# Optimization experiments

Hardware: AMD Instinct MI355X
Metric: run time of the kernel (lower is better)

The kernel has to match this reference:

```python
import jax, jax.numpy as jnp
import numpy as np

NUM_GRAPHS = 128
EPS = 1e-5


def _instance_norm(x, seg):
    # per-graph (segment) normalization over rows, per channel; affine=False (PyG default)
    ones = jnp.ones((x.shape[0],), x.dtype)
    cnt = jnp.maximum(jax.ops.segment_sum(ones, seg, num_segments=NUM_GRAPHS), 1.0)[:, None]
    mean = jax.ops.segment_sum(x, seg, num_segments=NUM_GRAPHS) / cnt
    ex2 = jax.ops.segment_sum(x * x, seg, num_segments=NUM_GRAPHS) / cnt
    var = jnp.maximum(ex2 - mean * mean, 0.0)
    return (x - mean[seg]) * jax.lax.rsqrt(var[seg] + EPS)


def setup_inputs() -> dict:
    key = jax.random.key(0)
    ks = jax.random.split(key, 6)
    N, E, H = 100_000, 1_600_000, 64
    emb = jax.random.normal(ks[0], (N, H), jnp.float32)
    edge_index = jax.random.randint(ks[1], (2, E), 0, N)
    batch = jnp.sort(jax.random.randint(ks[2], (N,), 0, NUM_GRAPHS))
    s = lambda fan: 1.0 / np.sqrt(fan)
    # MLP layers [2H, 4H, H, 1]
    W1 = jax.random.uniform(ks[3], (2 * H, 4 * H), jnp.float32, -s(2 * H), s(2 * H))
    b1 = jnp.zeros((4 * H,), jnp.float32)
    W2 = jax.random.uniform(ks[4], (4 * H, H), jnp.float32, -s(4 * H), s(4 * H))
    b2 = jnp.zeros((H,), jnp.float32)
    W3 = jax.random.uniform(ks[5], (H, 1), jnp.float32, -s(H), s(H))
    b3 = jnp.zeros((1,), jnp.float32)
    return dict(emb=emb, edge_index=edge_index, batch=batch,
                W1=W1, b1=b1, W2=W2, b2=b2, W3=W3, b3=b3)


def reference(emb, edge_index, batch, W1, b1, W2, b2, W3, b3):
    col, row = edge_index[0], edge_index[1]
    # edge-wise gather + concat: [E, 2H]
    f12 = jnp.concatenate([emb[col], emb[row]], axis=-1)
    seg = batch[col]  # graph id per edge
    h = jax.nn.relu(_instance_norm(f12 @ W1 + b1, seg))   # [E, 4H]
    h = jax.nn.relu(_instance_norm(h @ W2 + b2, seg))     # [E, H]
    att_log_logits = h @ W3 + b3                          # [E, 1]
    return att_log_logits
```

## Files before the change

### kernel.cpp

```cpp
#include <hip/hip_runtime.h>
#include <hip/hip_bf16.h>

#define NSEG 128
#define H64 64
#define C1 256
#define K1 128
#define C2 64
#define EPSV 1e-5f
#define NWG 256

typedef __attribute__((ext_vector_type(8))) short bf16x8;
typedef __attribute__((ext_vector_type(16))) float f32x16;
typedef __attribute__((ext_vector_type(4))) unsigned int u32x4;

struct BTrue  { static constexpr bool value = true; };
struct BFalse { static constexpr bool value = false; };

__device__ __forceinline__ unsigned short f2bf(float f){
  unsigned int x = __float_as_uint(f);
  x += 0x7fffu + ((x >> 16) & 1u);
  return (unsigned short)(x >> 16);
}
__device__ __forceinline__ float bf2f(unsigned short u){
  return __uint_as_float(((unsigned int)u) << 16);
}
__device__ __forceinline__ unsigned pkbf(float lo, float hi){
  unsigned r;
  asm("v_cvt_pk_bf16_f32 %0, %1, %2" : "=v"(r) : "v"(lo), "v"(hi));
  return r;
}
__device__ __forceinline__ bf16x8 mk8(unsigned a, unsigned b, unsigned c, unsigned d){
  u32x4 t = {a, b, c, d};
  return __builtin_bit_cast(bf16x8, t);
}
__device__ __forceinline__ int xcd_swz(int bid, int nwg){
  int q = nwg >> 3, r = nwg & 7;
  int x = bid & 7, o = bid >> 3;
  return (x < r ? x * (q + 1) : r * (q + 1) + (x - r) * q) + o;
}

__global__ void k_cvt_emb(const float* __restrict__ src, unsigned short* __restrict__ dst, int n4){
  int i = blockIdx.x * blockDim.x + threadIdx.x;
  if (i >= n4) return;
  float4 v = ((const float4*)src)[i];
  unsigned int a = (unsigned int)f2bf(v.x) | ((unsigned int)f2bf(v.y) << 16);
  unsigned int b = (unsigned int)f2bf(v.z) | ((unsigned int)f2bf(v.w) << 16);
  ((uint2*)dst)[i] = make_uint2(a, b);
}

__global__ void k_cvt_w(const float* __restrict__ W1, const float* __restrict__ W2,
                        unsigned short* __restrict__ W1T, unsigned short* __restrict__ W2T){
  int i = blockIdx.x * blockDim.x + threadIdx.x;
  if (i < C1 * K1){
    int c = i >> 7, k = i & 127;
    W1T[i] = f2bf(W1[k * C1 + c]);
  } else {
    int j = i - C1 * K1;
    if (j < C2 * C1){
      int c = j >> 8, k = j & 255;
      W2T[j] = f2bf(W2[k * C2 + c]);
    }
  }
}

__global__ void k_hist(const int* __restrict__ col, const int* __restrict__ batch,
                       int* __restrict__ segE, int* __restrict__ cnt, int E){
  __shared__ int h[NSEG];
  for (int i = threadIdx.x; i < NSEG; i += blockDim.x) h[i] = 0;
  __syncthreads();
  int stride = gridDim.x * blockDim.x;
  for (int e = blockIdx.x * blockDim.x + threadIdx.x; e < E; e += stride){
    int s = batch[col[e]];
    segE[e] = s;
    atomicAdd(&h[s], 1);
  }
  __syncthreads();
  for (int i = threadIdx.x; i < NSEG; i += blockDim.x)
    if (h[i]) atomicAdd(&cnt[i], h[i]);
}

__global__ void k_scan(const int* __restrict__ cnt, int* __restrict__ cursor,
                       float* __restrict__ cntf){
  if (threadIdx.x == 0){
    int acc = 0;
    for (int i = 0; i < NSEG; i++){ cursor[i] = acc; acc += cnt[i]; }
  }
  if (threadIdx.x < NSEG){
    int c = cnt[threadIdx.x];
    cntf[threadIdx.x] = (float)(c > 0 ? c : 1);
  }
}

__global__ void k_scatter(const int* __restrict__ segE, const int* __restrict__ ei,
                          int* __restrict__ cursor, int* __restrict__ perm,
                          int* __restrict__ segS, int* __restrict__ ecol, int* __restrict__ erow,
                          int* __restrict__ invp, int E, int epb){
  __shared__ int h[NSEG];
  __shared__ int base[NSEG];
  int b0 = blockIdx.x * epb;
  int b1 = b0 + epb < E ? b0 + epb : E;
  for (int i = threadIdx.x; i < NSEG; i += blockDim.x) h[i] = 0;
  __syncthreads();
  for (int e = b0 + threadIdx.x; e < b1; e += blockDim.x) atomicAdd(&h[segE[e]], 1);
  __syncthreads();
  for (int i = threadIdx.x; i < NSEG; i += blockDim.x)
    base[i] = h[i] ? atomicAdd(&cursor[i], h[i]) : 0;
  __syncthreads();
  for (int i = threadIdx.x; i < NSEG; i += blockDim.x) h[i] = 0;
  __syncthreads();
  for (int e = b0 + threadIdx.x; e < b1; e += blockDim.x){
    int s = segE[e];
    int p = base[s] + atomicAdd(&h[s], 1);
    perm[p] = e; segS[p] = s;
    ecol[p] = ei[e]; erow[p] = ei[(size_t)E + e];
    invp[e] = p;
  }
}

__global__ void __launch_bounds__(1024, 4)
k_stats1(const unsigned short* __restrict__ ebf, const unsigned short* __restrict__ W1T,
         const int* __restrict__ ecol, const int* __restrict__ erow, const int* __restrict__ segS,
         float* __restrict__ sum1, float* __restrict__ sq1, int NWT, int E, int T)
{
  __shared__ __align__(16) char wl[65536];
  {
    #pragma unroll
    for (int j = 0; j < 4; j++){
      int i = threadIdx.x + j * 1024;
      int r = i >> 4, u = i & 15;
      u32x4 v = *(const u32x4*)(W1T + (size_t)r * K1 + u * 8);
      *(u32x4*)(wl + r * 256 + ((u ^ (r & 15)) << 4)) = v;
    }
  }
  __syncthreads();

  const int lane = threadIdx.x & 63, w = threadIdx.x >> 6;
  const int g = lane >> 5, l31 = lane & 31;
  const int bid = xcd_swz(blockIdx.x, NWG);
  const int wt0 = (bid * 16 + w) * T;
  float psum[8] = {0,0,0,0,0,0,0,0}, psq[8] = {0,0,0,0,0,0,0,0};
  int cur = -1;

  auto flush = [&](int seg){
    if (seg < 0) return;
    #pragma unroll
    for (int nt = 0; nt < 8; nt++){
      float sv = psum[nt] + __shfl_xor(psum[nt], 32);
      float qv = psq[nt]  + __shfl_xor(psq[nt], 32);
      if (lane < 32){
        atomicAdd(&sum1[seg * C1 + nt * 32 + l31], sv);
        atomicAdd(&sq1 [seg * C1 + nt * 32 + l31], qv);
      }
      psum[nt] = 0.f; psq[nt] = 0.f;
    }
  };

  auto ld3 = [&](int wt, int& a, int& r, int& s){
    int e = wt * 32 + l31;
    int ec = e < E ? e : E - 1;
    a = ecol[ec]; r = erow[ec]; s = segS[ec];
  };

  int cA, rA, sg;
  if (wt0 < NWT) ld3(wt0, cA, rA, sg);

  for (int it = 0; it < T; ++it){
    int wt = wt0 + it;
    if (wt >= NWT) break;
    const int p0 = wt * 32;
    int nA, nR, nS;
    const bool hv = (it + 1 < T) && (wt + 1 < NWT);
    if (hv) ld3(wt + 1, nA, nR, nS);

    bf16x8 fa[8];
    #pragma unroll
    for (int kk = 0; kk < 8; kk++){
      int off = (kk & 3) * 16 + g * 8;
      fa[kk] = *(const bf16x8*)(ebf + (size_t)(kk < 4 ? cA : rA) * H64 + off);
    }

    int sA = __builtin_amdgcn_readfirstlane(__shfl(sg, 0));
    int sB = __builtin_amdgcn_readfirstlane(__shfl(sg, 31));
    bool uni = (sA == sB) && (p0 + 32 <= E);
    if (uni && sA != cur){ flush(cur); cur = sA; }
    if (!uni){ flush(cur); cur = -1; }

    #pragma unroll 1
    for (int np = 0; np < 4; np++){
      const int nt0 = 2 * np, nt1 = 2 * np + 1;
      f32x16 a0, a1;
      #pragma unroll
      for (int r = 0; r < 16; r++){ a0[r] = 0.f; a1[r] = 0.f; }
      const int rw0 = nt0 * 32 + l31, rw1 = nt1 * 32 + l31;
      __builtin_amdgcn_s_setprio(1);
      #pragma unroll
      for (int kk = 0; kk < 8; kk++){
        bf16x8 b0 = *(const bf16x8*)(wl + rw0 * 256 + (((2 * kk + g) ^ (rw0 & 15)) << 4));
        bf16x8 b1 = *(const bf16x8*)(wl + rw1 * 256 + (((2 * kk + g) ^ (rw1 & 15)) << 4));
        a0 = __builtin_amdgcn_mfma_f32_32x32x16_bf16(fa[kk], b0, a0, 0, 0, 0);
        a1 = __builtin_amdgcn_mfma_f32_32x32x16_bf16(fa[kk], b1, a1, 0, 0, 0);
      }
      __builtin_amdgcn_s_setprio(0);
      if (uni){
        float t0 = 0.f, q0 = 0.f, t1 = 0.f, q1 = 0.f;
        #pragma unroll
        for (int r = 0; r < 16; r++){
          t0 += a0[r]; q0 += a0[r] * a0[r];
          t1 += a1[r]; q1 += a1[r] * a1[r];
        }
        psum[nt0] += t0; psq[nt0] += q0;
        psum[nt1] += t1; psq[nt1] += q1;
      } else {
        for (int s = sA; s <= sB; s++){
          float t0 = 0.f, q0 = 0.f, t1 = 0.f, q1 = 0.f;
          #pragma unroll
          for (int r = 0; r < 16; r++){
            int c = (r & 3) + 8 * (r >> 2) + 4 * g;
            bool ok = (__shfl(sg, c) == s) && (p0 + c < E);
            float v0 = ok ? a0[r] : 0.f;
            float v1 = ok ? a1[r] : 0.f;
            t0 += v0; q0 += v0 * v0;
            t1 += v1; q1 += v1 * v1;
          }
          float s0 = t0 + __shfl_xor(t0, 32);
          float qq0 = q0 + __shfl_xor(q0, 32);
          float s1 = t1 + __shfl_xor(t1, 32);
          float qq1 = q1 + __shfl_xor(q1, 32);
          if (lane < 32){
            atomicAdd(&sum1[s * C1 + nt0 * 32 + l31], s0);
            atomicAdd(&sq1 [s * C1 + nt0 * 32 + l31], qq0);
            atomicAdd(&sum1[s * C1 + nt1 * 32 + l31], s1);
            atomicAdd(&sq1 [s * C1 + nt1 * 32 + l31], qq1);
          }
        }
      }
    }
    if (hv){ cA = nA; rA = nR; sg = nS; }
  }
  flush(cur);
}

__global__ void k_fin(const float* __restrict__ sum, const float* __restrict__ sq,
                      const float* __restrict__ cntf,
                      float* __restrict__ sc, float* __restrict__ sh, int C){
  int i = blockIdx.x * blockDim.x + threadIdx.x;
  if (i >= NSEG * C) return;
  int s = i / C;
  float c = cntf[s];
  float m = sum[i] / c;
  float v = fmaxf(sq[i] / c - m * m, 0.f);
  float inv = rsqrtf(v + EPSV);
  sc[i] = inv;
  sh[i] = -m * inv;
}

template<int MODE>
__global__ void __launch_bounds__(1024, 4)
k_mid(const unsigned short* __restrict__ ebf, const unsigned short* __restrict__ W1T,
      const unsigned short* __restrict__ W2T,
      const int* __restrict__ ecol, const int* __restrict__ erow,
      const int* __restrict__ segS, const int* __restrict__ perm,
      const float* __restrict__ sc1, const float* __restrict__ sh1,
      float* __restrict__ sum2, float* __restrict__ sq2,
      unsigned int* __restrict__ y2u,
      const float* __restrict__ sc2, const float* __restrict__ sh2,
      const float* __restrict__ W3, const float* __restrict__ b3,
      float* __restrict__ out, int NWT, int E, int T)
{
  __shared__ __align__(16) char wl[98304];
  __shared__ __align__(16) float scsh[16][512];
  {
    #pragma unroll
    for (int j = 0; j < 4; j++){
      int i = threadIdx.x + j * 1024;
      int r = i >> 4, u = i & 15;
      u32x4 v = *(const u32x4*)(W1T + (size_t)r * K1 + u * 8);
      *(u32x4*)(wl + r * 256 + ((u ^ (r & 15)) << 4)) = v;
    }
    #pragma unroll
    for (int j = 0; j < 2; j++){
      int i = threadIdx.x + j * 1024;
      int r = i >> 5, u = i & 31;
      u32x4 v = *(const u32x4*)(W2T + (size_t)r * C1 + u * 8);
      *(u32x4*)(wl + 65536 + r * 512 + ((u ^ (r & 31)) << 4)) = v;
    }
  }
  __syncthreads();

  const int lane = threadIdx.x & 63, w = threadIdx.x >> 6;
  const int g = lane >> 5, l31 = lane & 31;
  const int bid = xcd_swz(blockIdx.x, NWG);
  const int wt0 = (bid * 16 + w) * T;

  float b3v = 0.f;
  if (MODE == 2) b3v = b3[0];
  int wseg = -1;

  auto body = [&](auto uni_c, const bf16x8* fbp, int sgn, f32x16* acc2){
    constexpr bool UNI = decltype(uni_c)::value;
    #pragma unroll 1
    for (int mt = 0; mt < 8; mt++){
      f32x16 a1;
      #pragma unroll
      for (int r = 0; r < 16; r++) a1[r] = 0.f;
      const int rw = mt * 32 + l31;
      __builtin_amdgcn_s_setprio(1);
      #pragma unroll
      for (int kk = 0; kk < 8; kk++){
        bf16x8 wa = *(const bf16x8*)(wl + rw * 256 + (((2 * kk + g) ^ (rw & 15)) << 4));
        a1 = __builtin_amdgcn_mfma_f32_32x32x16_bf16(wa, fbp[kk], a1, 0, 0, 0);
      }
      __builtin_amdgcn_s_setprio(0);
      unsigned pk_[8];
      #pragma unroll
      for (int rq = 0; rq < 4; rq++){
        float4 sc, sh;
        if constexpr (UNI){
          sc = *(const float4*)(&scsh[w][mt * 32 + rq * 8 + 4 * g]);
          sh = *(const float4*)(&scsh[w][256 + mt * 32 + rq * 8 + 4 * g]);
        } else {
          sc = *(const float4*)(sc1 + sgn * C1 + mt * 32 + rq * 8 + 4 * g);
          sh = *(const float4*)(sh1 + sgn * C1 + mt * 32 + rq * 8 + 4 * g);
        }
        float h0 = fmaxf(fmaf(a1[rq * 4 + 0], sc.x, sh.x), 0.f);
        float h1 = fmaxf(fmaf(a1[rq * 4 + 1], sc.y, sh.y), 0.f);
        float h2 = fmaxf(fmaf(a1[rq * 4 + 2], sc.z, sh.z), 0.f);
        float h3 = fmaxf(fmaf(a1[rq * 4 + 3], sc.w, sh.w), 0.f);
        pk_[rq * 2 + 0] = pkbf(h0, h1);
        pk_[rq * 2 + 1] = pkbf(h2, h3);
      }
      asm("v_permlane32_swap_b32 %0, %1" : "+v"(pk_[0]), "+v"(pk_[2]));
      asm("v_permlane32_swap_b32 %0, %1" : "+v"(pk_[1]), "+v"(pk_[3]));
      asm("v_permlane32_swap_b32 %0, %1" : "+v"(pk_[4]), "+v"(pk_[6]));
      asm("v_permlane32_swap_b32 %0, %1" : "+v"(pk_[5]), "+v"(pk_[7]));
      bf16x8 bf0 = mk8(pk_[0], pk_[1], pk_[2], pk_[3]);
      bf16x8 bf1 = mk8(pk_[4], pk_[5], pk_[6], pk_[7]);
      __builtin_amdgcn_s_setprio(1);
      #pragma unroll
      for (int ct = 0; ct < 2; ct++){
        int rb = ct * 32 + l31;
        bf16x8 wb0 = *(const bf16x8*)(wl + 65536 + rb * 512 + (((4 * mt + g) ^ (rb & 31)) << 4));
        bf16x8 wb1 = *(const bf16x8*)(wl + 65536 + rb * 512 + (((4 * mt + 2 + g) ^ (rb & 31)) << 4));
        acc2[ct] = __builtin_amdgcn_mfma_f32_32x32x16_bf16(wb0, bf0, acc2[ct], 0, 0, 0);
        acc2[ct] = __builtin_amdgcn_mfma_f32_32x32x16_bf16(wb1, bf1, acc2[ct], 0, 0, 0);
      }
      __builtin_amdgcn_s_setprio(0);
    }
  };

  auto ld3 = [&](int wt, int& a, int& r, int& s){
    int e = wt * 32 + l31;
    int ec = e < E ? e : E - 1;
    a = ecol[ec]; r = erow[ec]; s = segS[ec];
  };

  int cA, rA, sg;
  if (wt0 < NWT) ld3(wt0, cA, rA, sg);

  for (int it = 0; it < T; ++it){
    int wt = wt0 + it;
    if (wt >= NWT) break;
    const int p0 = wt * 32;
    int nA, nR, nS;
    const bool hv = (it + 1 < T) && (wt + 1 < NWT);
    if (hv) ld3(wt + 1, nA, nR, nS);

    int e0 = p0 + l31;
    bool v0 = e0 < E;

    bf16x8 fb[8];
    #pragma unroll
    for (int kk = 0; kk < 8; kk++){
      int off = (kk & 3) * 16 + g * 8;
      fb[kk] = *(const bf16x8*)(ebf + (size_t)(kk < 4 ? cA : rA) * H64 + off);
    }

    int sA = __builtin_amdgcn_readfirstlane(__shfl(sg, 0));
    int sB = __builtin_amdgcn_readfirstlane(__shfl(sg, 31));
    const bool uni = (sA == sB) && (p0 + 32 <= E);

    if (uni && sA != wseg){
      float4 s4 = *(const float4*)(sc1 + sA * C1 + lane * 4);
      float4 h4 = *(const float4*)(sh1 + sA * C1 + lane * 4);
      *(float4*)(&scsh[w][lane * 4]) = s4;
      *(float4*)(&scsh[w][256 + lane * 4]) = h4;
      wseg = sA;
    }

    f32x16 acc2[2];
    #pragma unroll
    for (int ct = 0; ct < 2; ct++)
      #pragma unroll
      for (int r = 0; r < 16; r++) acc2[ct][r] = 0.f;

    if (uni) body(BTrue{},  fb, sg, acc2);
    else     body(BFalse{}, fb, sg, acc2);

    if constexpr (MODE == 0){
      if (v0){
        unsigned* yp = y2u + (size_t)e0 * 32;
        #pragma unroll
        for (int ct = 0; ct < 2; ct++)
          #pragma unroll
          for (int rq = 0; rq < 4; rq++){
            uint2 pv;
            pv.x = pkbf(acc2[ct][rq * 4 + 0], acc2[ct][rq * 4 + 1]);
            pv.y = pkbf(acc2[ct][rq * 4 + 2], acc2[ct][rq * 4 + 3]);
            *(uint2*)(yp + ct * 16 + rq * 4 + 2 * g) = pv;
          }
      }
      for (int s = sA; s <= sB; s++){
        #pragma unroll
        for (int ct = 0; ct < 2; ct++)
          #pragma unroll
          for (int r = 0; r < 16; r++){
            float x = (v0 && sg == s) ? acc2[ct][r] : 0.f;
            float vs = x, vq = x * x;
            #pragma unroll
            for (int off = 1; off < 32; off <<= 1){
              vs += __shfl_xor(vs, off);
              vq += __shfl_xor(vq, off);
            }
            if (l31 == 0){
              int c2 = ct * 32 + (r & 3) + 8 * (r >> 2) + 4 * g;
              atomicAdd(&sum2[s * C2 + c2], vs);
              atomicAdd(&sq2 [s * C2 + c2], vq);
            }
          }
      }
    } else if constexpr (MODE == 1){
      for (int s = sA; s <= sB; s++){
        #pragma unroll
        for (int ct = 0; ct < 2; ct++)
          #pragma unroll
          for (int r = 0; r < 16; r++){
            float x = (v0 && sg == s) ? acc2[ct][r] : 0.f;
            float vs = x, vq = x * x;
            #pragma unroll
            for (int off = 1; off < 32; off <<= 1){
              vs += __shfl_xor(vs, off);
              vq += __shfl_xor(vq, off);
            }
            if (l31 == 0){
              int c2 = ct * 32 + (r & 3) + 8 * (r >> 2) + 4 * g;
              atomicAdd(&sum2[s * C2 + c2], vs);
              atomicAdd(&sq2 [s * C2 + c2], vq);
            }
          }
      }
    } else {
      float acc = 0.f;
      #pragma unroll
      for (int ct = 0; ct < 2; ct++)
        #pragma unroll
        for (int rq = 0; rq < 4; rq++){
          float4 sc = *(const float4*)(sc2 + sg * C2 + ct * 32 + rq * 8 + 4 * g);
          float4 sh = *(const float4*)(sh2 + sg * C2 + ct * 32 + rq * 8 + 4 * g);
          float4 wq = *(const float4*)(W3 + ct * 32 + rq * 8 + 4 * g);
          acc = fmaf(fmaxf(fmaf(acc2[ct][rq * 4 + 0], sc.x, sh.x), 0.f), wq.x, acc);
          acc = fmaf(fmaxf(fmaf(acc2[ct][rq * 4 + 1], sc.y, sh.y), 0.f), wq.y, acc);
          acc = fmaf(fmaxf(fmaf(acc2[ct][rq * 4 + 2], sc.z, sh.z), 0.f), wq.z, acc);
          acc = fmaf(fmaxf(fmaf(acc2[ct][rq * 4 + 3], sc.w, sh.w), 0.f), wq.w, acc);
        }
      acc += __shfl_xor(acc, 32);
      if (g == 0 && v0) out[perm[e0]] = acc + b3v;
    }
    if (hv){ cA = nA; rA = nR; sg = nS; }
  }
}

__global__ void k_out(const unsigned short* __restrict__ y2, const int* __restrict__ segS,
                      const float* __restrict__ sc2, const float* __restrict__ sh2,
                      const float* __restrict__ W3, const float* __restrict__ b3,
                      float* __restrict__ tmp, int E)
{
  const int lane = threadIdx.x & 63;
  const int wid = (blockIdx.x * blockDim.x + threadIdx.x) >> 6;
  const int nw = (gridDim.x * blockDim.x) >> 6;
  const int es = lane >> 3;
  const int cp = (lane & 7) * 8;
  float w3r[8];
  #pragma unroll
  for (int j = 0; j < 8; j++) w3r[j] = W3[cp + j];
  const float b3v = b3[0];
  for (long base = (long)wid * 8; base < E; base += (long)nw * 8){
    int pos = (int)base + es;
    float a = 0.f;
    if (pos < E){
      bf16x8 v = *(const bf16x8*)(y2 + (size_t)pos * C2 + cp);
      int s = segS[pos];
      const float* scp = sc2 + s * C2 + cp;
      const float* shp = sh2 + s * C2 + cp;
      #pragma unroll
      for (int j = 0; j < 8; j++){
        float hv = fmaxf(fmaf(bf2f((unsigned short)v[j]), scp[j], shp[j]), 0.f);
        a = fmaf(hv, w3r[j], a);
      }
    }
    a += __shfl_xor(a, 1); a += __shfl_xor(a, 2); a += __shfl_xor(a, 4);
    if ((lane & 7) == 0 && pos < E) tmp[pos] = a + b3v;
  }
}

__global__ void k_remap(const float* __restrict__ tmp, const int* __restrict__ invp,
                        float* __restrict__ out, int E)
{
  int stride = gridDim.x * blockDim.x;
  for (int e = blockIdx.x * blockDim.x + threadIdx.x; e < E; e += stride)
    out[e] = tmp[invp[e]];
}

extern "C" void kernel_launch(void* const* d_in, const int* in_sizes, int n_in,
                              void* d_out, int out_size, void* d_ws, size_t ws_size,
                              hipStream_t stream)
{
  const float* emb   = (const float*)d_in[0];
  const int*   ei    = (const int*)d_in[1];
  const int*   batch = (const int*)d_in[2];
  const float* W1    = (const float*)d_in[3];
  const float* W2    = (const float*)d_in[5];
  const float* W3    = (const float*)d_in[7];
  const float* b3    = (const float*)d_in[8];
  float* out = (float*)d_out;
  const int E = in_sizes[1] / 2;
  const int N = in_sizes[0] / H64;
  const int NWT = (E + 31) / 32;

  char* ws = (char*)d_ws;
  size_t o = 0;
  auto al = [&](size_t b){ size_t r = o; o = (o + b + 255) & ~((size_t)255); return r; };
  size_t o_ebf  = al((size_t)N * H64 * 2);
  size_t o_w1t  = al((size_t)C1 * K1 * 2);
  size_t o_w2t  = al((size_t)C2 * C1 * 2);
  size_t o_perm = al((size_t)E * 4);
  size_t o_segS = al((size_t)E * 4);
  size_t o_ecol = al((size_t)E * 4);
  size_t o_erow = al((size_t)E * 4);
  size_t o_invp = al((size_t)E * 4);
  size_t o_cnt  = al(NSEG * 4);
  size_t o_cur  = al(NSEG * 4);
  size_t o_cntf = al(NSEG * 4);
  size_t o_sum1 = al((size_t)NSEG * C1 * 4);
  size_t o_sq1  = al((size_t)NSEG * C1 * 4);
  size_t o_sum2 = al((size_t)NSEG * C2 * 4);
  size_t o_sq2  = al((size_t)NSEG * C2 * 4);
  size_t o_sc1  = al((size_t)NSEG * C1 * 4);
  size_t o_sh1  = al((size_t)NSEG * C1 * 4);
  size_t o_sc2  = al((size_t)NSEG * C2 * 4);
  size_t o_sh2  = al((size_t)NSEG * C2 * 4);
  size_t o_segE = al((size_t)E * 4);
  size_t o_y2   = o_segE;
  size_t need_full = o_segE + (size_t)E * C2 * 2;
  const bool full = ws_size >= need_full;

  unsigned short* ebf = (unsigned short*)(ws + o_ebf);
  unsigned short* W1T = (unsigned short*)(ws + o_w1t);
  unsigned short* W2T = (unsigned short*)(ws + o_w2t);
  int* perm = (int*)(ws + o_perm);
  int* segS = (int*)(ws + o_segS);
  int* ecol = (int*)(ws + o_ecol);
  int* erow = (int*)(ws + o_erow);
  int* invp = (int*)(ws + o_invp);
  int* cnt  = (int*)(ws + o_cnt);
  int* curp = (int*)(ws + o_cur);
  float* cntf = (float*)(ws + o_cntf);
  float* sum1 = (float*)(ws + o_sum1);
  float* sq1  = (float*)(ws + o_sq1);
  float* sum2 = (float*)(ws + o_sum2);
  float* sq2  = (float*)(ws + o_sq2);
  float* sc1  = (float*)(ws + o_sc1);
  float* sh1  = (float*)(ws + o_sh1);
  float* sc2  = (float*)(ws + o_sc2);
  float* sh2  = (float*)(ws + o_sh2);
  int* segE = (int*)(ws + o_segE);
  unsigned int* y2u = (unsigned int*)(ws + o_y2);
  unsigned short* y2 = (unsigned short*)(ws + o_y2);
  float* tmp = (float*)(ws + o_ecol);

  hipMemsetAsync(ws + o_cnt, 0, o_sc1 - o_cnt, stream);

  k_cvt_emb<<<(N * H64 / 4 + 255) / 256, 256, 0, stream>>>(emb, ebf, N * H64 / 4);
  k_cvt_w<<<192, 256, 0, stream>>>(W1, W2, W1T, W2T);

  k_hist<<<2048, 256, 0, stream>>>(ei, batch, segE, cnt, E);
  k_scan<<<1, 128, 0, stream>>>(cnt, curp, cntf);
  const int epb = 2048;
  k_scatter<<<(E + epb - 1) / epb, 256, 0, stream>>>(segE, ei, curp, perm, segS, ecol, erow, invp, E, epb);

  const int T = (NWT + NWG * 16 - 1) / (NWG * 16);
  k_stats1<<<NWG, 1024, 0, stream>>>(ebf, W1T, ecol, erow, segS, sum1, sq1, NWT, E, T);
  k_fin<<<(NSEG * C1) / 256, 256, 0, stream>>>(sum1, sq1, cntf, sc1, sh1, C1);

  if (full){
    k_mid<0><<<NWG, 1024, 0, stream>>>(ebf, W1T, W2T, ecol, erow, segS, perm,
        sc1, sh1, sum2, sq2, y2u, sc2, sh2, W3, b3, out, NWT, E, T);
    k_fin<<<(NSEG * C2) / 256, 256, 0, stream>>>(sum2, sq2, cntf, sc2, sh2, C2);
    k_out<<<1024, 256, 0, stream>>>(y2, segS, sc2, sh2, W3, b3, tmp, E);
    k_remap<<<2048, 256, 0, stream>>>(tmp, invp, out, E);
  } else {
    k_mid<1><<<NWG, 1024, 0, stream>>>(ebf, W1T, W2T, ecol, erow, segS, perm,
        sc1, sh1, sum2, sq2, nullptr, sc2, sh2, W3, b3, out, NWT, E, T);
    k_fin<<<(NSEG * C2) / 256, 256, 0, stream>>>(sum2, sq2, cntf, sc2, sh2, C2);
    k_mid<2><<<NWG, 1024, 0, stream>>>(ebf, W1T, W2T, ecol, erow, segS, perm,
        sc1, sh1, sum2, sq2, nullptr, sc2, sh2, W3, b3, out, NWT, E, T);
  }
}
```

Before: 658.7 us.

## Transpose second MFMA so edges lie in rows and accumulate segment stats in registers

Result: faster. 565.6 us (-14.1%).

```diff
diff --git a/kernel.cpp b/kernel.cpp
--- a/kernel.cpp
+++ b/kernel.cpp
@@ -295,6 +295,22 @@
   float b3v = 0.f;
   if (MODE == 2) b3v = b3[0];
   int wseg = -1;
+  float ps2[2] = {0.f, 0.f}, pq2[2] = {0.f, 0.f};
+  int cur2 = -1;
+
+  auto flush2 = [&](int seg){
+    if (seg < 0) return;
+    #pragma unroll
+    for (int ct = 0; ct < 2; ct++){
+      float sv = ps2[ct] + __shfl_xor(ps2[ct], 32);
+      float qv = pq2[ct] + __shfl_xor(pq2[ct], 32);
+      if (lane < 32){
+        atomicAdd(&sum2[seg * C2 + ct * 32 + l31], sv);
+        atomicAdd(&sq2 [seg * C2 + ct * 32 + l31], qv);
+      }
+      ps2[ct] = 0.f; pq2[ct] = 0.f;
+    }
+  };
 
   auto body = [&](auto uni_c, const bf16x8* fbp, int sgn, f32x16* acc2){
     constexpr bool UNI = decltype(uni_c)::value;
@@ -341,8 +357,8 @@
         int rb = ct * 32 + l31;
         bf16x8 wb0 = *(const bf16x8*)(wl + 65536 + rb * 512 + (((4 * mt + g) ^ (rb & 31)) << 4));
         bf16x8 wb1 = *(const bf16x8*)(wl + 65536 + rb * 512 + (((4 * mt + 2 + g) ^ (rb & 31)) << 4));
-        acc2[ct] = __builtin_amdgcn_mfma_f32_32x32x16_bf16(wb0, bf0, acc2[ct], 0, 0, 0);
-        acc2[ct] = __builtin_amdgcn_mfma_f32_32x32x16_bf16(wb1, bf1, acc2[ct], 0, 0, 0);
+        acc2[ct] = __builtin_amdgcn_mfma_f32_32x32x16_bf16(bf0, wb0, acc2[ct], 0, 0, 0);
+        acc2[ct] = __builtin_amdgcn_mfma_f32_32x32x16_bf16(bf1, wb1, acc2[ct], 0, 0, 0);
       }
       __builtin_amdgcn_s_setprio(0);
     }
@@ -365,9 +381,6 @@
     const bool hv = (it + 1 < T) && (wt + 1 < NWT);
     if (hv) ld3(wt + 1, nA, nR, nS);
 
-    int e0 = p0 + l31;
-    bool v0 = e0 < E;
-
     bf16x8 fb[8];
     #pragma unroll
     for (int kk = 0; kk < 8; kk++){
@@ -396,77 +409,71 @@
     if (uni) body(BTrue{},  fb, sg, acc2);
     else     body(BFalse{}, fb, sg, acc2);
 
-    if constexpr (MODE == 0){
-      if (v0){
-        unsigned* yp = y2u + (size_t)e0 * 32;
+    if constexpr (MODE < 2){
+      if constexpr (MODE == 0){
+        unsigned short* y2s = (unsigned short*)y2u;
         #pragma unroll
-        for (int ct = 0; ct < 2; ct++)
-          #pragma unroll
-          for (int rq = 0; rq < 4; rq++){
-            uint2 pv;
-            pv.x = pkbf(acc2[ct][rq * 4 + 0], acc2[ct][rq * 4 + 1]);
-            pv.y = pkbf(acc2[ct][rq * 4 + 2], acc2[ct][rq * 4 + 3]);
-            *(uint2*)(yp + ct * 16 + rq * 4 + 2 * g) = pv;
-          }
-      }
-      for (int s = sA; s <= sB; s++){
-        #pragma unroll
-        for (int ct = 0; ct < 2; ct++)
+        for (int ct = 0; ct < 2; ct++){
+          int ch = ct * 32 + l31;
           #pragma unroll
           for (int r = 0; r < 16; r++){
-            float x = (v0 && sg == s) ? acc2[ct][r] : 0.f;
-            float vs = x, vq = x * x;
+            int eloc = (r & 3) + 8 * (r >> 2) + 4 * g;
+            if (p0 + eloc < E)
+              y2s[(size_t)(p0 + eloc) * C2 + ch] = f2bf(acc2[ct][r]);
+          }
+        }
+      }
+      if (uni){
+        if (sA != cur2){ flush2(cur2); cur2 = sA; }
+        #pragma unroll
+        for (int ct = 0; ct < 2; ct++){
+          float ts = 0.f, tq = 0.f;
+          #pragma unroll
+          for (int r = 0; r < 16; r++){ float x = acc2[ct][r]; ts += x; tq += x * x; }
+          ps2[ct] += ts; pq2[ct] += tq;
+        }
+      } else {
+        flush2(cur2); cur2 = -1;
+        for (int s = sA; s <= sB; s++){
+          #pragma unroll
+          for (int ct = 0; ct < 2; ct++){
+            float ts = 0.f, tq = 0.f;
             #pragma unroll
-            for (int off = 1; off < 32; off <<= 1){
-              vs += __shfl_xor(vs, off);
-              vq += __shfl_xor(vq, off);
+            for (int r = 0; r < 16; r++){
+              int eloc = (r & 3) + 8 * (r >> 2) + 4 * g;
+              bool ok = (__shfl(sg, eloc) == s) && (p0 + eloc < E);
+              float x = ok ? acc2[ct][r] : 0.f;
+              ts += x; tq += x * x;
             }
-            if (l31 == 0){
-              int c2 = ct * 32 + (r & 3) + 8 * (r >> 2) + 4 * g;
-              atomicAdd(&sum2[s * C2 + c2], vs);
-              atomicAdd(&sq2 [s * C2 + c2], vq);
+            float sv = ts + __shfl_xor(ts, 32);
+            float qv = tq + __shfl_xor(tq, 32);
+            if (lane < 32){
+              atomicAdd(&sum2[s * C2 + ct * 32 + l31], sv);
+              atomicAdd(&sq2 [s * C2 + ct * 32 + l31], qv);
             }
           }
-      }
-    } else if constexpr (MODE == 1){
-      for (int s = sA; s <= sB; s++){
+        }
+      }
+    } else {
+      #pragma unroll
+      for (int r = 0; r < 16; r++){
+        int eloc = (r & 3) + 8 * (r >> 2) + 4 * g;
+        int sge = uni ? sA : __shfl(sg, eloc);
+        float vtot = 0.f;
         #pragma unroll
-        for (int ct = 0; ct < 2; ct++)
-          #pragma unroll
-          for (int r = 0; r < 16; r++){
-            float x = (v0 && sg == s) ? acc2[ct][r] : 0.f;
-            float vs = x, vq = x * x;
-            #pragma unroll
-            for (int off = 1; off < 32; off <<= 1){
-              vs += __shfl_xor(vs, off);
-              vq += __shfl_xor(vq, off);
-            }
-            if (l31 == 0){
-              int c2 = ct * 32 + (r & 3) + 8 * (r >> 2) + 4 * g;
-              atomicAdd(&sum2[s * C2 + c2], vs);
-              atomicAdd(&sq2 [s * C2 + c2], vq);
-            }
-          }
-      }
-    } else {
-      float acc = 0.f;
-      #pragma unroll
-      for (int ct = 0; ct < 2; ct++)
-        #pragma unroll
-        for (int rq = 0; rq < 4; rq++){
-          float4 sc = *(const float4*)(sc2 + sg * C2 + ct * 32 + rq * 8 + 4 * g);
-          float4 sh = *(const float4*)(sh2 + sg * C2 + ct * 32 + rq * 8 + 4 * g);
-          float4 wq = *(const float4*)(W3 + ct * 32 + rq * 8 + 4 * g);
-          acc = fmaf(fmaxf(fmaf(acc2[ct][rq * 4 + 0], sc.x, sh.x), 0.f), wq.x, acc);
-          acc = fmaf(fmaxf(fmaf(acc2[ct][rq * 4 + 1], sc.y, sh.y), 0.f), wq.y, acc);
-          acc = fmaf(fmaxf(fmaf(acc2[ct][rq * 4 + 2], sc.z, sh.z), 0.f), wq.z, acc);
-          acc = fmaf(fmaxf(fmaf(acc2[ct][rq * 4 + 3], sc.w, sh.w), 0.f), wq.w, acc);
+        for (int ct = 0; ct < 2; ct++){
+          int ch = ct * 32 + l31;
+          float scv = sc2[sge * C2 + ch], shv = sh2[sge * C2 + ch];
+          vtot += fmaxf(fmaf(acc2[ct][r], scv, shv), 0.f) * W3[ch];
         }
-      acc += __shfl_xor(acc, 32);
-      if (g == 0 && v0) out[perm[e0]] = acc + b3v;
+        vtot += __shfl_xor(vtot, 1); vtot += __shfl_xor(vtot, 2);
+        vtot += __shfl_xor(vtot, 4); vtot += __shfl_xor(vtot, 8); vtot += __shfl_xor(vtot, 16);
+        if (l31 == 0 && p0 + eloc < E) out[perm[p0 + eloc]] = vtot + b3v;
+      }
     }
     if (hv){ cA = nA; rA = nR; sg = nS; }
   }
+  if constexpr (MODE < 2) flush2(cur2);
 }
 
 __global__ void k_out(const unsigned short* __restrict__ y2, const int* __restrict__ segS,
```
